# Optimization experiments

Hardware: AMD Instinct MI355X
Metric: run time of the kernel (lower is better)

Reference implementation:

```python
import jax, jax.numpy as jnp
import numpy as np

N, C, X, H = 50000, 8, 256, 256

def setup_inputs() -> dict:
    key = jax.random.key(0)
    k1, k2, k3, k4, k5, k6 = jax.random.split(key, 6)
    child_h = jax.random.normal(k1, (N, C, X), dtype=jnp.float32)
    parent_h = jax.random.normal(k2, (N, X), dtype=jnp.float32)
    u = lambda k, s: jax.random.uniform(k, s, jnp.float32, -0.1, 0.1)
    return {
        "child_h": child_h,
        "parent_h": parent_h,
        "W_left": u(k3, (X, H)),
        "W_right": u(k4, (X, H)),
        "W_top": u(k5, (X, H)),
        "b_conv": u(k6, (1, H)),
    }

def reference(child_h, parent_h, W_left, W_right, W_top, b_conv):
    # Positional continuous-binary-tree weights over C children:
    #   left_w[i]  = (C-1-i)/(C-1),  right_w[i] = i/(C-1)
    C_ = child_h.shape[1]
    i = jnp.arange(C_, dtype=child_h.dtype)
    left_w = (C_ - 1 - i) / (C_ - 1)   # [C]
    right_w = i / (C_ - 1)             # [C]
    # sum_i lw_i*(h_i @ W_l) + rw_i*(h_i @ W_r) == (sum_i lw_i h_i) @ W_l + (sum_i rw_i h_i) @ W_r
    s_left = jnp.einsum("ncx,c->nx", child_h, left_w)    # [N, X]
    s_right = jnp.einsum("ncx,c->nx", child_h, right_w)  # [N, X]
    children_state = s_left @ W_left + s_right @ W_right  # [N, H]
    return jax.nn.relu(children_state + parent_h @ W_top + b_conv)
```

## Files before the change

kernel.cpp:

```cpp
#include <hip/hip_runtime.h>
#include <hip/hip_bf16.h>

#define NROWS 50000
#define CDIM 8
#define XDIM 256
#define HDIM 256

typedef __attribute__((ext_vector_type(8))) short bf16x8;
typedef __attribute__((ext_vector_type(4))) float f32x4;

__device__ __forceinline__ unsigned short f2bf_rne(float f) {
    unsigned int u = __builtin_bit_cast(unsigned int, f);
    u += 0x7fffu + ((u >> 16) & 1u);
    return (unsigned short)(u >> 16);
}

__device__ __forceinline__ bf16x8 pack8(const f32x4 a, const f32x4 b) {
    bf16x8 r;
    r[0] = (short)f2bf_rne(a[0]);
    r[1] = (short)f2bf_rne(a[1]);
    r[2] = (short)f2bf_rne(a[2]);
    r[3] = (short)f2bf_rne(a[3]);
    r[4] = (short)f2bf_rne(b[0]);
    r[5] = (short)f2bf_rne(b[1]);
    r[6] = (short)f2bf_rne(b[2]);
    r[7] = (short)f2bf_rne(b[3]);
    return r;
}

__global__ __launch_bounds__(256) void pack_weights(
        const float* __restrict__ Wl, const float* __restrict__ Wr,
        const float* __restrict__ Wt, bf16x8* __restrict__ wp) {
    int t = blockIdx.x * 256 + threadIdx.x;
    int lane = t & 63;
    int tile = t >> 6;
    int ht  = tile & 15;
    int sx  = tile >> 4;
    int xc  = sx & 7;
    int seg = sx >> 3;
    const float* __restrict__ W = (seg == 0) ? Wl : (seg == 1) ? Wr : Wt;
    int x0 = xc * 32 + (lane >> 4) * 8;
    int h  = ht * 16 + (lane & 15);
    bf16x8 frag;
#pragma unroll
    for (int j = 0; j < 8; ++j)
        frag[j] = (short)f2bf_rne(W[(size_t)(x0 + j) * HDIM + h]);
    wp[t] = frag;
}

__global__ __launch_bounds__(256) void tbcnn_main(
        const float* __restrict__ child, const float* __restrict__ parent,
        const bf16x8* __restrict__ wp, const float* __restrict__ bias,
        float* __restrict__ out) {
    __shared__ bf16x8 flds[2][4][3][64];

    const int wave = threadIdx.x >> 6;
    const int lane = threadIdx.x & 63;
    const int rmod = lane & 15;
    const int quad = lane >> 4;

    const int blk0   = blockIdx.x * 64;
    const int rb_own = blk0 + wave * 16;
    const int row_own = ((rb_own + 16 <= NROWS) ? rb_own : (NROWS - 16)) + rmod;

    const float* __restrict__ chrow = child  + (size_t)row_own * (CDIM * XDIM);
    const float* __restrict__ prow  = parent + (size_t)row_own * XDIM;

    const float lwt[8] = {7.f/7.f, 6.f/7.f, 5.f/7.f, 4.f/7.f, 3.f/7.f, 2.f/7.f, 1.f/7.f, 0.f/7.f};
    const float rwt[8] = {0.f/7.f, 1.f/7.f, 2.f/7.f, 3.f/7.f, 4.f/7.f, 5.f/7.f, 6.f/7.f, 7.f/7.f};

    f32x4 acc[4][4];
#pragma unroll
    for (int rt = 0; rt < 4; ++rt)
#pragma unroll
        for (int t = 0; t < 4; ++t) acc[rt][t] = (f32x4){0.f, 0.f, 0.f, 0.f};

    bf16x8 wn[4];
    {
        const bf16x8* wb0 = wp + (size_t)((0 * 16 + wave * 4) * 64 + lane);
#pragma unroll
        for (int t = 0; t < 4; ++t) wn[t] = wb0[t * 64];
    }

#pragma unroll 1
    for (int xc = 0; xc < 8; ++xc) {
        const int p  = xc & 1;
        const int x0 = xc * 32 + quad * 8;
        const bf16x8* wb = wp + (size_t)((xc * 16 + wave * 4) * 64 + lane);

        f32x4 sl0 = (f32x4){0.f,0.f,0.f,0.f}, sl1 = (f32x4){0.f,0.f,0.f,0.f};
        f32x4 sr0 = (f32x4){0.f,0.f,0.f,0.f}, sr1 = (f32x4){0.f,0.f,0.f,0.f};
#pragma unroll
        for (int c = 0; c < CDIM; ++c) {
            const f32x4* cp = (const f32x4*)(chrow + (size_t)c * XDIM + x0);
            f32x4 a = cp[0];
            f32x4 b = cp[1];
            sl0 += a * lwt[c];  sl1 += b * lwt[c];
            sr0 += a * rwt[c];  sr1 += b * rwt[c];
        }
        const f32x4* pp = (const f32x4*)(prow + x0);
        f32x4 p0 = pp[0];
        f32x4 p1 = pp[1];

        flds[p][wave][0][lane] = pack8(sl0, sl1);
        flds[p][wave][1][lane] = pack8(sr0, sr1);
        flds[p][wave][2][lane] = pack8(p0, p1);
        __syncthreads();

#pragma unroll
        for (int seg = 0; seg < 3; ++seg) {
            bf16x8 wc[4];
#pragma unroll
            for (int t = 0; t < 4; ++t) wc[t] = wn[t];
            const int noff = (seg < 2) ? (seg + 1) * 8192 : 1024;
#pragma unroll
            for (int t = 0; t < 4; ++t) wn[t] = wb[noff + t * 64];
#pragma unroll
            for (int rt = 0; rt < 4; ++rt) {
                bf16x8 f = flds[p][rt][seg][lane];
#pragma unroll
                for (int t = 0; t < 4; ++t)
                    acc[rt][t] = __builtin_amdgcn_mfma_f32_16x16x32_bf16(wc[t], f, acc[rt][t], 0, 0, 0);
            }
        }
    }

#pragma unroll
    for (int rt = 0; rt < 4; ++rt) {
        const int rb = blk0 + rt * 16;
        if (rb + 16 <= NROWS) {
            float* __restrict__ orow = out + (size_t)(rb + rmod) * HDIM;
#pragma unroll
            for (int t = 0; t < 4; ++t) {
                const int h = (wave * 4 + t) * 16 + quad * 4;
                f32x4 b4 = *(const f32x4*)(bias + h);
                f32x4 v = acc[rt][t];
                v[0] = fmaxf(v[0] + b4[0], 0.f);
                v[1] = fmaxf(v[1] + b4[1], 0.f);
                v[2] = fmaxf(v[2] + b4[2], 0.f);
                v[3] = fmaxf(v[3] + b4[3], 0.f);
                *(f32x4*)(orow + h) = v;
            }
        }
    }
}

__global__ __launch_bounds__(256) void tbcnn_fallback(
        const float* __restrict__ child, const float* __restrict__ parent,
        const float* __restrict__ Wl, const float* __restrict__ Wr,
        const float* __restrict__ Wt, const float* __restrict__ bias,
        float* __restrict__ out) {
    __shared__ float sl[XDIM], sr[XDIM], sp[XDIM];
    const int n = blockIdx.x;
    const int h = threadIdx.x;
    const float lwt[8] = {7.f/7.f, 6.f/7.f, 5.f/7.f, 4.f/7.f, 3.f/7.f, 2.f/7.f, 1.f/7.f, 0.f/7.f};
    const float rwt[8] = {0.f/7.f, 1.f/7.f, 2.f/7.f, 3.f/7.f, 4.f/7.f, 5.f/7.f, 6.f/7.f, 7.f/7.f};
    const float* ch = child + (size_t)n * (CDIM * XDIM);
    float al = 0.f, ar = 0.f;
#pragma unroll
    for (int c = 0; c < CDIM; ++c) {
        float v = ch[c * XDIM + h];
        al += lwt[c] * v;
        ar += rwt[c] * v;
    }
    sl[h] = al; sr[h] = ar; sp[h] = parent[(size_t)n * XDIM + h];
    __syncthreads();
    float a = bias[h];
    for (int x = 0; x < XDIM; ++x)
        a += sl[x] * Wl[(size_t)x * HDIM + h] + sr[x] * Wr[(size_t)x * HDIM + h]
           + sp[x] * Wt[(size_t)x * HDIM + h];
    out[(size_t)n * HDIM + h] = fmaxf(a, 0.f);
}

extern "C" void kernel_launch(void* const* d_in, const int* in_sizes, int n_in,
                              void* d_out, int out_size, void* d_ws, size_t ws_size,
                              hipStream_t stream) {
    const float* child  = (const float*)d_in[0];
    const float* parent = (const float*)d_in[1];
    const float* Wl     = (const float*)d_in[2];
    const float* Wr     = (const float*)d_in[3];
    const float* Wt     = (const float*)d_in[4];
    const float* bias   = (const float*)d_in[5];
    float* out = (float*)d_out;

    const size_t wp_bytes = (size_t)3 * XDIM * HDIM * sizeof(unsigned short);
    if (ws_size >= wp_bytes) {
        bf16x8* wp = (bf16x8*)d_ws;
        pack_weights<<<96, 256, 0, stream>>>(Wl, Wr, Wt, wp);
        const int n_blocks = (NROWS + 63) / 64;
        tbcnn_main<<<n_blocks, 256, 0, stream>>>(child, parent, wp, bias, out);
    } else {
        tbcnn_fallback<<<NROWS, 256, 0, stream>>>(child, parent, Wl, Wr, Wt, bias, out);
    }
}
```

Measured before the change: 612.4 us.

## Stream child tiles into LDS asynchronously with double buffering, 16 rows per block

Each block now handles 16 rows instead of 64. The next x-chunk of child_h is prefetched straight into a double-buffered LDS tile with global_load_lds, behind manual waitcnt and barriers, so memory latency overlaps the MFMA work. The child reduction is split across all four waves reading swizzled LDS, and weight fragments are loaded directly per segment rather than register-prefetched. This trades weight reuse across row tiles (weights are now reloaded per 16 rows) for more blocks and better overlap of the dominant child_h stream. It also relies on NROWS being divisible by 16.

```diff
diff --git a/kernel.cpp b/kernel.cpp
--- a/kernel.cpp
+++ b/kernel.cpp
@@ -1,5 +1,4 @@
 #include <hip/hip_runtime.h>
-#include <hip/hip_bf16.h>
 
 #define NROWS 50000
 #define CDIM 8
@@ -8,24 +7,15 @@
 
 typedef __attribute__((ext_vector_type(8))) short bf16x8;
 typedef __attribute__((ext_vector_type(4))) float f32x4;
+typedef __attribute__((ext_vector_type(2))) float f32x2;
 
 __device__ __forceinline__ unsigned short f2bf_rne(float f) {
     unsigned int u = __builtin_bit_cast(unsigned int, f);
     u += 0x7fffu + ((u >> 16) & 1u);
     return (unsigned short)(u >> 16);
 }
-
-__device__ __forceinline__ bf16x8 pack8(const f32x4 a, const f32x4 b) {
-    bf16x8 r;
-    r[0] = (short)f2bf_rne(a[0]);
-    r[1] = (short)f2bf_rne(a[1]);
-    r[2] = (short)f2bf_rne(a[2]);
-    r[3] = (short)f2bf_rne(a[3]);
-    r[4] = (short)f2bf_rne(b[0]);
-    r[5] = (short)f2bf_rne(b[1]);
-    r[6] = (short)f2bf_rne(b[2]);
-    r[7] = (short)f2bf_rne(b[3]);
-    return r;
+__device__ __forceinline__ unsigned int pack2(float lo, float hi) {
+    return (unsigned int)f2bf_rne(lo) | ((unsigned int)f2bf_rne(hi) << 16);
 }
 
 __global__ __launch_bounds__(256) void pack_weights(
@@ -48,100 +38,112 @@
     wp[t] = frag;
 }
 
-__global__ __launch_bounds__(256) void tbcnn_main(
+__global__ __launch_bounds__(256, 3) void tbcnn_main(
         const float* __restrict__ child, const float* __restrict__ parent,
         const bf16x8* __restrict__ wp, const float* __restrict__ bias,
         float* __restrict__ out) {
-    __shared__ bf16x8 flds[2][4][3][64];
+    __shared__ __align__(16) float chlds[2][CDIM][2][8][8][4];
+    __shared__ __align__(16) bf16x8 flds[2][3 * 64];
 
-    const int wave = threadIdx.x >> 6;
-    const int lane = threadIdx.x & 63;
-    const int rmod = lane & 15;
-    const int quad = lane >> 4;
+    const int tid  = threadIdx.x;
+    const int wave = tid >> 6;
+    const int lane = tid & 63;
+    const int r    = lane & 15;
+    const int p2   = lane >> 4;
+    const int blk16 = blockIdx.x * 16;
 
-    const int blk0   = blockIdx.x * 64;
-    const int rb_own = blk0 + wave * 16;
-    const int row_own = ((rb_own + 16 <= NROWS) ? rb_own : (NROWS - 16)) + rmod;
-
-    const float* __restrict__ chrow = child  + (size_t)row_own * (CDIM * XDIM);
-    const float* __restrict__ prow  = parent + (size_t)row_own * XDIM;
+    const int row8 = lane >> 3;
+    const int slot = lane & 7;
+    const int gch  = slot ^ row8;
 
     const float lwt[8] = {7.f/7.f, 6.f/7.f, 5.f/7.f, 4.f/7.f, 3.f/7.f, 2.f/7.f, 1.f/7.f, 0.f/7.f};
     const float rwt[8] = {0.f/7.f, 1.f/7.f, 2.f/7.f, 3.f/7.f, 4.f/7.f, 5.f/7.f, 6.f/7.f, 7.f/7.f};
 
-    f32x4 acc[4][4];
+    f32x4 acc[4];
 #pragma unroll
-    for (int rt = 0; rt < 4; ++rt)
+    for (int t = 0; t < 4; ++t) acc[t] = (f32x4){0.f, 0.f, 0.f, 0.f};
+
+    f32x2 pnxt;
+    {
 #pragma unroll
-        for (int t = 0; t < 4; ++t) acc[rt][t] = (f32x4){0.f, 0.f, 0.f, 0.f};
-
-    bf16x8 wn[4];
-    {
-        const bf16x8* wb0 = wp + (size_t)((0 * 16 + wave * 4) * 64 + lane);
-#pragma unroll
-        for (int t = 0; t < 4; ++t) wn[t] = wb0[t * 64];
+        for (int k = 0; k < 4; ++k) {
+            const int i = k * 4 + wave;
+            const int c = i >> 1, rh = i & 1;
+            const float* src = child + (size_t)(blk16 + rh * 8 + row8) * (CDIM * XDIM)
+                             + c * XDIM + 0 * 32 + gch * 4;
+            __builtin_amdgcn_global_load_lds(
+                (const __attribute__((address_space(1))) unsigned int*)src,
+                (__attribute__((address_space(3))) unsigned int*)&chlds[0][c][rh][0][0][0],
+                16, 0, 0);
+        }
+        pnxt = *(const f32x2*)(parent + (size_t)(blk16 + r) * XDIM + 0 * 32 + wave * 8 + p2 * 2);
     }
 
 #pragma unroll 1
     for (int xc = 0; xc < 8; ++xc) {
-        const int p  = xc & 1;
-        const int x0 = xc * 32 + quad * 8;
-        const bf16x8* wb = wp + (size_t)((xc * 16 + wave * 4) * 64 + lane);
+        const int cb = xc & 1;
+        const f32x2 pcur = pnxt;
 
-        f32x4 sl0 = (f32x4){0.f,0.f,0.f,0.f}, sl1 = (f32x4){0.f,0.f,0.f,0.f};
-        f32x4 sr0 = (f32x4){0.f,0.f,0.f,0.f}, sr1 = (f32x4){0.f,0.f,0.f,0.f};
+        if (xc < 7) {
 #pragma unroll
-        for (int c = 0; c < CDIM; ++c) {
-            const f32x4* cp = (const f32x4*)(chrow + (size_t)c * XDIM + x0);
-            f32x4 a = cp[0];
-            f32x4 b = cp[1];
-            sl0 += a * lwt[c];  sl1 += b * lwt[c];
-            sr0 += a * rwt[c];  sr1 += b * rwt[c];
+            for (int k = 0; k < 4; ++k) {
+                const int i = k * 4 + wave;
+                const int c = i >> 1, rh = i & 1;
+                const float* src = child + (size_t)(blk16 + rh * 8 + row8) * (CDIM * XDIM)
+                                 + c * XDIM + (xc + 1) * 32 + gch * 4;
+                __builtin_amdgcn_global_load_lds(
+                    (const __attribute__((address_space(1))) unsigned int*)src,
+                    (__attribute__((address_space(3))) unsigned int*)&chlds[cb ^ 1][c][rh][0][0][0],
+                    16, 0, 0);
+            }
+            pnxt = *(const f32x2*)(parent + (size_t)(blk16 + r) * XDIM + (xc + 1) * 32 + wave * 8 + p2 * 2);
+            asm volatile("s_waitcnt vmcnt(5)" ::: "memory");
+        } else {
+            asm volatile("s_waitcnt vmcnt(0)" ::: "memory");
         }
-        const f32x4* pp = (const f32x4*)(prow + x0);
-        f32x4 p0 = pp[0];
-        f32x4 p1 = pp[1];
+        __builtin_amdgcn_s_barrier();
+        asm volatile("" ::: "memory");
 
-        flds[p][wave][0][lane] = pack8(sl0, sl1);
-        flds[p][wave][1][lane] = pack8(sr0, sr1);
-        flds[p][wave][2][lane] = pack8(p0, p1);
-        __syncthreads();
+        {
+            const int rh_r = r >> 3, r8 = r & 7;
+            const int sl_  = (wave * 2 + (p2 >> 1)) ^ r8;
+            const int sub  = (p2 & 1) * 2;
+            float sl0 = 0.f, sl1 = 0.f, sr0 = 0.f, sr1 = 0.f;
+#pragma unroll
+            for (int c = 0; c < CDIM; ++c) {
+                f32x2 a = *(const f32x2*)&chlds[cb][c][rh_r][r8][sl_][sub];
+                sl0 += a[0] * lwt[c];  sl1 += a[1] * lwt[c];
+                sr0 += a[0] * rwt[c];  sr1 += a[1] * rwt[c];
+            }
+            ((unsigned int*)&flds[cb][0 * 64 + wave * 16 + r])[p2] = pack2(sl0, sl1);
+            ((unsigned int*)&flds[cb][1 * 64 + wave * 16 + r])[p2] = pack2(sr0, sr1);
+            ((unsigned int*)&flds[cb][2 * 64 + wave * 16 + r])[p2] = pack2(pcur[0], pcur[1]);
+        }
+        asm volatile("s_waitcnt lgkmcnt(0)" ::: "memory");
+        __builtin_amdgcn_s_barrier();
+        asm volatile("" ::: "memory");
 
 #pragma unroll
         for (int seg = 0; seg < 3; ++seg) {
-            bf16x8 wc[4];
+            const bf16x8* wb = wp + ((size_t)((seg * 8 + xc) * 16 + wave * 4)) * 64 + lane;
+            bf16x8 f = flds[cb][seg * 64 + lane];
 #pragma unroll
-            for (int t = 0; t < 4; ++t) wc[t] = wn[t];
-            const int noff = (seg < 2) ? (seg + 1) * 8192 : 1024;
-#pragma unroll
-            for (int t = 0; t < 4; ++t) wn[t] = wb[noff + t * 64];
-#pragma unroll
-            for (int rt = 0; rt < 4; ++rt) {
-                bf16x8 f = flds[p][rt][seg][lane];
-#pragma unroll
-                for (int t = 0; t < 4; ++t)
-                    acc[rt][t] = __builtin_amdgcn_mfma_f32_16x16x32_bf16(wc[t], f, acc[rt][t], 0, 0, 0);
-            }
+            for (int t = 0; t < 4; ++t)
+                acc[t] = __builtin_amdgcn_mfma_f32_16x16x32_bf16(wb[t * 64], f, acc[t], 0, 0, 0);
         }
     }
 
+    float* __restrict__ orow = out + (size_t)(blk16 + r) * HDIM;
 #pragma unroll
-    for (int rt = 0; rt < 4; ++rt) {
-        const int rb = blk0 + rt * 16;
-        if (rb + 16 <= NROWS) {
-            float* __restrict__ orow = out + (size_t)(rb + rmod) * HDIM;
-#pragma unroll
-            for (int t = 0; t < 4; ++t) {
-                const int h = (wave * 4 + t) * 16 + quad * 4;
-                f32x4 b4 = *(const f32x4*)(bias + h);
-                f32x4 v = acc[rt][t];
-                v[0] = fmaxf(v[0] + b4[0], 0.f);
-                v[1] = fmaxf(v[1] + b4[1], 0.f);
-                v[2] = fmaxf(v[2] + b4[2], 0.f);
-                v[3] = fmaxf(v[3] + b4[3], 0.f);
-                *(f32x4*)(orow + h) = v;
-            }
-        }
+    for (int t = 0; t < 4; ++t) {
+        const int h = (wave * 4 + t) * 16 + p2 * 4;
+        f32x4 b4 = *(const f32x4*)(bias + h);
+        f32x4 v = acc[t];
+        v[0] = fmaxf(v[0] + b4[0], 0.f);
+        v[1] = fmaxf(v[1] + b4[1], 0.f);
+        v[2] = fmaxf(v[2] + b4[2], 0.f);
+        v[3] = fmaxf(v[3] + b4[3], 0.f);
+        *(f32x4*)(orow + h) = v;
     }
 }
 
@@ -187,7 +189,7 @@
     if (ws_size >= wp_bytes) {
         bf16x8* wp = (bf16x8*)d_ws;
         pack_weights<<<96, 256, 0, stream>>>(Wl, Wr, Wt, wp);
-        const int n_blocks = (NROWS + 63) / 64;
+        const int n_blocks = NROWS / 16;
         tbcnn_main<<<n_blocks, 256, 0, stream>>>(child, parent, wp, bias, out);
     } else {
         tbcnn_fallback<<<NROWS, 256, 0, stream>>>(child, parent, Wl, Wr, Wt, bias, out);
```

Result: no change. 604.5 us (-1.3%).
